# Kernel optimization log

Measured on AMD Instinct MI355X. Metric: run time of the kernel, lower is better.

## Reference

```python
import jax, jax.numpy as jnp
import numpy as np

L = 512        # cfg.DATASET.SQUARE_IMAGE_LENGTH
SIGMA = 8.0    # cfg.DATASET.SIGMA
TRUNC = 4.6052 # exp(-4.6052) ~= 0.01, standard CPM truncation


def setup_inputs() -> dict:
    key = jax.random.key(0)
    k1, k2, k3 = jax.random.split(key, 3)
    B, N, H, W = 32, 17, 128, 128
    heatmaps_predict = jax.random.normal(k1, (B, N, H, W), dtype=jnp.float32)
    # labels in [-1, 1)
    kp_labels = jax.random.uniform(k2, (B, N, 2), dtype=jnp.float32) * 2.0 - 1.0
    kp_mask = jax.random.randint(k3, (B, N), 0, 2).astype(jnp.float32)
    return {"heatmaps_predict": heatmaps_predict, "kp_labels": kp_labels, "kp_mask": kp_mask}


def _gaussian_maps(centers, H, W, stride):
    # centers: [B, N, 2] with (x, y) in pixel coords of the full image.
    start = stride / 2.0 - 0.5
    gx = start + jnp.arange(W, dtype=jnp.float32) * stride  # [W]
    gy = start + jnp.arange(H, dtype=jnp.float32) * stride  # [H]
    cx = centers[..., 0][..., None, None]  # [B, N, 1, 1]
    cy = centers[..., 1][..., None, None]
    d2 = (gx[None, None, None, :] - cx) ** 2 + (gy[None, None, :, None] - cy) ** 2  # [B,N,H,W]
    expo = d2 / (2.0 * SIGMA * SIGMA)
    return jnp.where(expo > TRUNC, 0.0, jnp.exp(-expo))


def reference(heatmaps_predict, kp_labels, kp_mask):
    B, N, H, W = heatmaps_predict.shape
    stride = L // W
    valid = (kp_mask > 0).astype(heatmaps_predict.dtype)  # [B, N]
    num_valid = jnp.sum(kp_mask)
    centers = jnp.clip((kp_labels / 2.0 + 0.5) * L, 0.0, L - 1.0)  # [B, N, 2]
    heatmap_gt = _gaussian_maps(centers, H, W, stride)              # [B, N, H, W]
    per_kp_loss = jnp.mean((heatmaps_predict - heatmap_gt) ** 2, axis=(2, 3))  # [B, N]
    total = jnp.sum(per_kp_loss * valid)
    denom = jnp.maximum(num_valid, 1.0)
    return jnp.where(num_valid > 0, total / denom, jnp.array(0.0, heatmaps_predict.dtype))
```

## Files before the change

kernel.cpp:

```cpp
#include <hip/hip_runtime.h>

constexpr int   B  = 32, N = 17;
constexpr int   BN = B * N;
constexpr int   H = 128, W = 128, HW = H * W;
constexpr int   BLOCKS_PER_BN = 4;
constexpr int   NPART = BN * BLOCKS_PER_BN;
constexpr float L_IMG   = 512.0f;
constexpr float STRIDE  = 4.0f;
constexpr float START   = STRIDE / 2.0f - 0.5f;
constexpr float INV2SG2 = 1.0f / (2.0f * 8.0f * 8.0f);
constexpr float TRUNCV  = 4.6052f;

__global__ __launch_bounds__(256)
void heatmap_loss_per_kp(const float* __restrict__ pred,
                         const float* __restrict__ labels,
                         const float* __restrict__ mask,
                         float* __restrict__ part)
{
    const int bid = blockIdx.x;
    const int bn  = bid >> 2;
    const int q   = bid & 3;
    const int t   = threadIdx.x;

    const float lx = labels[bn * 2 + 0];
    const float ly = labels[bn * 2 + 1];
    const float cx = fminf(fmaxf((lx * 0.5f + 0.5f) * L_IMG, 0.0f), L_IMG - 1.0f);
    const float cy = fminf(fmaxf((ly * 0.5f + 0.5f) * L_IMG, 0.0f), L_IMG - 1.0f);

    const float4* p4 = reinterpret_cast<const float4*>(pred + (size_t)bn * HW) + q * 1024;

    float acc = 0.0f;
    #pragma unroll
    for (int j = 0; j < 4; ++j) {
        const int f4 = j * 256 + t;
        const float4 v = p4[f4];
        const int e = (q * 1024 + f4) * 4;
        const int h = e >> 7;
        const int w = e & 127;
        const float dy  = fmaf(STRIDE, (float)h, START) - cy;
        const float dy2 = dy * dy;

        const float pv[4] = { v.x, v.y, v.z, v.w };
        #pragma unroll
        for (int k = 0; k < 4; ++k) {
            const float dx   = fmaf(STRIDE, (float)(w + k), START) - cx;
            const float d2   = fmaf(dx, dx, dy2);
            const float expo = d2 * INV2SG2;
            const float gt   = (expo > TRUNCV) ? 0.0f : __expf(-expo);
            const float diff = pv[k] - gt;
            acc = fmaf(diff, diff, acc);
        }
    }

    #pragma unroll
    for (int off = 32; off > 0; off >>= 1)
        acc += __shfl_down(acc, off, 64);

    __shared__ float sacc[4];
    const int wave = t >> 6;
    if ((t & 63) == 0) sacc[wave] = acc;
    __syncthreads();

    if (t == 0) {
        const float s     = sacc[0] + sacc[1] + sacc[2] + sacc[3];
        const float valid = (mask[bn] > 0.0f) ? 1.0f : 0.0f;
        part[bid] = s * (1.0f / (float)HW) * valid;
    }
}

__global__ __launch_bounds__(256)
void heatmap_loss_final(const float* __restrict__ part,
                        const float* __restrict__ mask,
                        float* __restrict__ out)
{
    const int t = threadIdx.x;
    float tot = 0.0f, nv = 0.0f;
    #pragma unroll
    for (int i = t; i < NPART; i += 256) tot += part[i];
    for (int i = t; i < BN;    i += 256) nv  += mask[i];
    #pragma unroll
    for (int off = 32; off > 0; off >>= 1) {
        tot += __shfl_down(tot, off, 64);
        nv  += __shfl_down(nv,  off, 64);
    }
    __shared__ float st[4], sn[4];
    const int wave = t >> 6;
    if ((t & 63) == 0) { st[wave] = tot; sn[wave] = nv; }
    __syncthreads();
    if (t == 0) {
        const float T  = st[0] + st[1] + st[2] + st[3];
        const float NV = sn[0] + sn[1] + sn[2] + sn[3];
        out[0] = (NV > 0.0f) ? (T / fmaxf(NV, 1.0f)) : 0.0f;
    }
}

extern "C" void kernel_launch(void* const* d_in, const int* in_sizes, int n_in,
                              void* d_out, int out_size, void* d_ws, size_t ws_size,
                              hipStream_t stream) {
    const float* pred   = (const float*)d_in[0];
    const float* labels = (const float*)d_in[1];
    const float* mask   = (const float*)d_in[2];
    float* out = (float*)d_out;
    float* ws  = (float*)d_ws;

    heatmap_loss_per_kp<<<NPART, 256, 0, stream>>>(pred, labels, mask, ws);
    heatmap_loss_final<<<1, 256, 0, stream>>>(ws, mask, out);
}
```

Baseline: 13.29 us.

## Skip loads for masked keypoints and fuse final reduction via last-block counter

Blocks whose keypoint mask is zero skip reading predictions and computing the Gaussian, since their contribution is zeroed anyway. The separate final reduction kernel is replaced by an atomic counter so the last finishing block sums the partials. This roughly halves memory traffic for random masks. It adds a memset launch and threadfence/atomic synchronisation.

```diff
diff --git a/kernel.cpp b/kernel.cpp
--- a/kernel.cpp
+++ b/kernel.cpp
@@ -12,85 +12,84 @@
 constexpr float TRUNCV  = 4.6052f;
 
 __global__ __launch_bounds__(256)
-void heatmap_loss_per_kp(const float* __restrict__ pred,
-                         const float* __restrict__ labels,
-                         const float* __restrict__ mask,
-                         float* __restrict__ part)
+void heatmap_loss_fused(const float* __restrict__ pred,
+                        const float* __restrict__ labels,
+                        const float* __restrict__ mask,
+                        float* __restrict__ part,
+                        unsigned int* __restrict__ counter,
+                        float* __restrict__ out)
 {
     const int bid = blockIdx.x;
     const int bn  = bid >> 2;
     const int q   = bid & 3;
     const int t   = threadIdx.x;
-
-    const float lx = labels[bn * 2 + 0];
-    const float ly = labels[bn * 2 + 1];
-    const float cx = fminf(fmaxf((lx * 0.5f + 0.5f) * L_IMG, 0.0f), L_IMG - 1.0f);
-    const float cy = fminf(fmaxf((ly * 0.5f + 0.5f) * L_IMG, 0.0f), L_IMG - 1.0f);
-
-    const float4* p4 = reinterpret_cast<const float4*>(pred + (size_t)bn * HW) + q * 1024;
+    const int wave = t >> 6;
 
     float acc = 0.0f;
-    #pragma unroll
-    for (int j = 0; j < 4; ++j) {
-        const int f4 = j * 256 + t;
-        const float4 v = p4[f4];
-        const int e = (q * 1024 + f4) * 4;
-        const int h = e >> 7;
-        const int w = e & 127;
-        const float dy  = fmaf(STRIDE, (float)h, START) - cy;
-        const float dy2 = dy * dy;
+    if (mask[bn] > 0.0f) {
+        const float lx = labels[bn * 2 + 0];
+        const float ly = labels[bn * 2 + 1];
+        const float cx = fminf(fmaxf((lx * 0.5f + 0.5f) * L_IMG, 0.0f), L_IMG - 1.0f);
+        const float cy = fminf(fmaxf((ly * 0.5f + 0.5f) * L_IMG, 0.0f), L_IMG - 1.0f);
 
-        const float pv[4] = { v.x, v.y, v.z, v.w };
+        const float4* p4 = reinterpret_cast<const float4*>(pred + (size_t)bn * HW) + q * 1024;
+
         #pragma unroll
-        for (int k = 0; k < 4; ++k) {
-            const float dx   = fmaf(STRIDE, (float)(w + k), START) - cx;
-            const float d2   = fmaf(dx, dx, dy2);
-            const float expo = d2 * INV2SG2;
-            const float gt   = (expo > TRUNCV) ? 0.0f : __expf(-expo);
-            const float diff = pv[k] - gt;
-            acc = fmaf(diff, diff, acc);
+        for (int j = 0; j < 4; ++j) {
+            const int f4 = j * 256 + t;
+            const float4 v = p4[f4];
+            const int e = (q * 1024 + f4) * 4;
+            const int h = e >> 7;
+            const int w = e & 127;
+            const float dy  = fmaf(STRIDE, (float)h, START) - cy;
+            const float dy2 = dy * dy;
+            const float pv[4] = { v.x, v.y, v.z, v.w };
+            #pragma unroll
+            for (int k = 0; k < 4; ++k) {
+                const float dx   = fmaf(STRIDE, (float)(w + k), START) - cx;
+                const float d2   = fmaf(dx, dx, dy2);
+                const float expo = d2 * INV2SG2;
+                const float gt   = (expo > TRUNCV) ? 0.0f : __expf(-expo);
+                const float diff = pv[k] - gt;
+                acc = fmaf(diff, diff, acc);
+            }
         }
+        #pragma unroll
+        for (int off = 32; off > 0; off >>= 1)
+            acc += __shfl_down(acc, off, 64);
     }
 
-    #pragma unroll
-    for (int off = 32; off > 0; off >>= 1)
-        acc += __shfl_down(acc, off, 64);
-
     __shared__ float sacc[4];
-    const int wave = t >> 6;
+    __shared__ int   s_last;
     if ((t & 63) == 0) sacc[wave] = acc;
     __syncthreads();
 
     if (t == 0) {
-        const float s     = sacc[0] + sacc[1] + sacc[2] + sacc[3];
-        const float valid = (mask[bn] > 0.0f) ? 1.0f : 0.0f;
-        part[bid] = s * (1.0f / (float)HW) * valid;
+        part[bid] = (sacc[0] + sacc[1] + sacc[2] + sacc[3]) * (1.0f / (float)HW);
+        __threadfence();
+        const unsigned int old = atomicAdd(counter, 1u);
+        s_last = (old == (unsigned int)(NPART - 1)) ? 1 : 0;
     }
-}
+    __syncthreads();
 
-__global__ __launch_bounds__(256)
-void heatmap_loss_final(const float* __restrict__ part,
-                        const float* __restrict__ mask,
-                        float* __restrict__ out)
-{
-    const int t = threadIdx.x;
-    float tot = 0.0f, nv = 0.0f;
-    #pragma unroll
-    for (int i = t; i < NPART; i += 256) tot += part[i];
-    for (int i = t; i < BN;    i += 256) nv  += mask[i];
-    #pragma unroll
-    for (int off = 32; off > 0; off >>= 1) {
-        tot += __shfl_down(tot, off, 64);
-        nv  += __shfl_down(nv,  off, 64);
-    }
-    __shared__ float st[4], sn[4];
-    const int wave = t >> 6;
-    if ((t & 63) == 0) { st[wave] = tot; sn[wave] = nv; }
-    __syncthreads();
-    if (t == 0) {
-        const float T  = st[0] + st[1] + st[2] + st[3];
-        const float NV = sn[0] + sn[1] + sn[2] + sn[3];
-        out[0] = (NV > 0.0f) ? (T / fmaxf(NV, 1.0f)) : 0.0f;
+    if (s_last) {
+        __threadfence();
+        float tot = 0.0f, nv = 0.0f;
+        for (int i = t; i < NPART; i += 256) tot += part[i];
+        for (int i = t; i < BN;    i += 256) nv  += mask[i];
+        #pragma unroll
+        for (int off = 32; off > 0; off >>= 1) {
+            tot += __shfl_down(tot, off, 64);
+            nv  += __shfl_down(nv,  off, 64);
+        }
+        __shared__ float st[4], sn[4];
+        if ((t & 63) == 0) { st[wave] = tot; sn[wave] = nv; }
+        __syncthreads();
+        if (t == 0) {
+            const float T  = st[0] + st[1] + st[2] + st[3];
+            const float NV = sn[0] + sn[1] + sn[2] + sn[3];
+            out[0] = (NV > 0.0f) ? (T / fmaxf(NV, 1.0f)) : 0.0f;
+        }
     }
 }
 
@@ -101,8 +100,10 @@
     const float* labels = (const float*)d_in[1];
     const float* mask   = (const float*)d_in[2];
     float* out = (float*)d_out;
-    float* ws  = (float*)d_ws;
 
-    heatmap_loss_per_kp<<<NPART, 256, 0, stream>>>(pred, labels, mask, ws);
-    heatmap_loss_final<<<1, 256, 0, stream>>>(ws, mask, out);
+    float*        part    = (float*)d_ws;
+    unsigned int* counter = (unsigned int*)((char*)d_ws + NPART * sizeof(float));
+
+    hipMemsetAsync(counter, 0, sizeof(unsigned int), stream);
+    heatmap_loss_fused<<<NPART, 256, 0, stream>>>(pred, labels, mask, part, counter, out);
 }
```

After: 52.89 us. 3.98x slower.
